# Performance work log

Hardware: AMD Instinct MI355X
Metric: run time of the kernel (lower is better)

Reference implementation:

```python
import jax, jax.numpy as jnp
import numpy as np

NUM_HEADS = 16
ROPE_THETA = 10000.0


def _rope_cos_sin(seq_len, head_dim, dtype):
    # Llama rotary embedding: inv_freq over even dims, emb = cat(freqs, freqs)
    inv_freq = 1.0 / (ROPE_THETA ** (jnp.arange(0, head_dim, 2, dtype=jnp.float32) / head_dim))
    t = jnp.arange(seq_len, dtype=jnp.float32)
    freqs = jnp.outer(t, inv_freq)              # [S, hd/2]
    emb = jnp.concatenate([freqs, freqs], -1)   # [S, hd]
    return jnp.cos(emb).astype(dtype), jnp.sin(emb).astype(dtype)


def _rotate_half(x):
    h = x.shape[-1] // 2
    return jnp.concatenate([-x[..., h:], x[..., :h]], axis=-1)


def setup_inputs() -> dict:
    key = jax.random.key(0)
    ks = jax.random.split(key, 5)
    B, S, D = 1, 2048, 2048
    scale = 0.02
    return {
        "hidden_states": jax.random.normal(ks[0], (B, S, D), jnp.float32),
        "Wq": jax.random.normal(ks[1], (D, D), jnp.float32) * scale,
        "Wk": jax.random.normal(ks[2], (D, D), jnp.float32) * scale,
        "Wv": jax.random.normal(ks[3], (D, D), jnp.float32) * scale,
        "Wo": jax.random.normal(ks[4], (D, D), jnp.float32) * scale,
    }


def reference(hidden_states, Wq, Wk, Wv, Wo):
    B, S, D = hidden_states.shape
    H = NUM_HEADS
    hd = D // H
    sm_scale = 1.0 / np.sqrt(hd)

    # QKV projections (nn.Linear without bias: x @ W.T), kept in [B,S,H,hd]
    q = (hidden_states @ Wq.T).reshape(B, S, H, hd)
    k = (hidden_states @ Wk.T).reshape(B, S, H, hd)
    v = (hidden_states @ Wv.T).reshape(B, S, H, hd)

    # RoPE (offset=0, no kv cache)
    cos, sin = _rope_cos_sin(S, hd, hidden_states.dtype)
    cos = cos[None, :, None, :]  # [1,S,1,hd]
    sin = sin[None, :, None, :]
    q = q * cos + _rotate_half(q) * sin
    k = k * cos + _rotate_half(k) * sin

    # Causal self-attention (exact math of FlashSelfAttention(causal=True))
    scores = jnp.einsum("bshd,bthd->bhst", q, k) * sm_scale  # [B,H,S,S]
    causal = jnp.tril(jnp.ones((S, S), dtype=bool))
    scores = jnp.where(causal[None, None], scores, jnp.finfo(scores.dtype).min)
    probs = jax.nn.softmax(scores, axis=-1)
    attn = jnp.einsum("bhst,bthd->bshd", probs, v)           # [B,S,H,hd]

    # Output projection
    attn = attn.reshape(B, S, H * hd)
    return attn @ Wo.T
```

## Files before the change

### kernel.cpp

```cpp
#include <hip/hip_runtime.h>
#include <hip/hip_bf16.h>
#include <math.h>

#define S_LEN 2048
#define DMODEL 2048
#define NHEADS 16
#define HDIM 128

typedef __bf16 bf16x8 __attribute__((ext_vector_type(8)));
typedef float f32x4 __attribute__((ext_vector_type(4)));
typedef float f32x16 __attribute__((ext_vector_type(16)));

__device__ __forceinline__ unsigned short f2b(float f) {
  union { float f; unsigned u; } c; c.f = f;
  unsigned r = (c.u + 0x7fffu + ((c.u >> 16) & 1u)) >> 16;
  return (unsigned short)r;
}
__device__ __forceinline__ float b2f(unsigned short b) {
  union { unsigned u; float f; } c; c.u = ((unsigned)b) << 16;
  return c.f;
}

__device__ __forceinline__ void gload_lds16(const unsigned short* g, unsigned short* l) {
  __builtin_amdgcn_global_load_lds(
      (__attribute__((address_space(1))) void*)(void*)g,
      (__attribute__((address_space(3))) void*)(void*)l, 16, 0, 0);
}

__global__ void cvt5_f32_bf16_k(const float* __restrict__ s0,
                                const float* __restrict__ s1,
                                const float* __restrict__ s2,
                                const float* __restrict__ s3,
                                const float* __restrict__ s4,
                                unsigned short* __restrict__ d0,
                                unsigned short* __restrict__ d1,
                                unsigned short* __restrict__ d2,
                                unsigned short* __restrict__ d3,
                                unsigned short* __restrict__ d4) {
  int gi = blockIdx.x * blockDim.x + threadIdx.x;
  int seg = gi >> 20;
  int i = (gi & 0xFFFFF) * 4;
  const float* src = (seg == 0) ? s0 : (seg == 1) ? s1 : (seg == 2) ? s2
                     : (seg == 3) ? s3 : s4;
  unsigned short* dst = (seg == 0) ? d0 : (seg == 1) ? d1 : (seg == 2) ? d2
                        : (seg == 3) ? d3 : d4;
  float4 v = *reinterpret_cast<const float4*>(src + i);
  ushort4 o;
  o.x = f2b(v.x); o.y = f2b(v.y); o.z = f2b(v.z); o.w = f2b(v.w);
  *reinterpret_cast<ushort4*>(dst + i) = o;
}

__global__ void rope_table_k(float* __restrict__ cs, float* __restrict__ sn) {
  int idx = blockIdx.x * blockDim.x + threadIdx.x;
  int s = idx >> 6, i = idx & 63;
  float inv = powf(10000.0f, -(float)(2 * i) / 128.0f);
  float a = (float)s * inv;
  cs[idx] = cosf(a);
  sn[idx] = sinf(a);
}

__global__ void rope_apply_k(unsigned short* __restrict__ q,
                             unsigned short* __restrict__ k,
                             const float* __restrict__ cs,
                             const float* __restrict__ sn) {
  const float SC = 0.08838834764831845f * 1.4426950408889634f;
  int idx = blockIdx.x * blockDim.x + threadIdx.x;
  int i = idx & 63;
  int h = (idx >> 6) & (NHEADS - 1);
  int s = idx >> 10;
  size_t base = (size_t)s * DMODEL + h * HDIM;
  float c = cs[s * 64 + i], sv = sn[s * 64 + i];
  float qc = c * SC, qs = sv * SC;
  float q1 = b2f(q[base + i]), q2 = b2f(q[base + i + 64]);
  q[base + i]      = f2b(q1 * qc - q2 * qs);
  q[base + i + 64] = f2b(q2 * qc + q1 * qs);
  float k1 = b2f(k[base + i]), k2 = b2f(k[base + i + 64]);
  k[base + i]      = f2b(k1 * c - k2 * sv);
  k[base + i + 64] = f2b(k2 * c + k1 * sv);
}

__global__ __launch_bounds__(256) void transpose_bf16_k(
    const unsigned short* __restrict__ in, unsigned short* __restrict__ out) {
  __shared__ unsigned short tile[64][72];
  int bx = blockIdx.x, by = blockIdx.y;
  int t = threadIdx.x;
#pragma unroll
  for (int i = 0; i < 2; ++i) {
    int ch = i * 256 + t;
    int r = ch >> 3, c8 = ch & 7;
    bf16x8 v = *reinterpret_cast<const bf16x8*>(
        in + (size_t)(by * 64 + r) * DMODEL + bx * 64 + c8 * 8);
    *reinterpret_cast<bf16x8*>(&tile[r][c8 * 8]) = v;
  }
  __syncthreads();
#pragma unroll
  for (int i = 0; i < 2; ++i) {
    int ch = i * 256 + t;
    int c = ch >> 3, r8 = ch & 7;
    union { bf16x8 v; unsigned short u[8]; } w;
#pragma unroll
    for (int j = 0; j < 8; ++j) w.u[j] = tile[r8 * 8 + j][c];
    *reinterpret_cast<bf16x8*>(
        out + (size_t)(bx * 64 + c) * S_LEN + by * 64 + r8 * 8) = w.v;
  }
}


#define MIDBAR_SEQ()                                      \
  do {                                                    \
    asm volatile("" ::: "memory");                        \
    __builtin_amdgcn_s_barrier();                         \
    asm volatile("s_waitcnt lgkmcnt(0)" ::: "memory");    \
    __builtin_amdgcn_sched_barrier(0);                    \
    __builtin_amdgcn_s_setprio(1);                        \
  } while (0)

#define ENDBAR_SEQ()                                      \
  do {                                                    \
    __builtin_amdgcn_s_setprio(0);                        \
    asm volatile("" ::: "memory");                        \
    __builtin_amdgcn_s_barrier();                         \
    asm volatile("" ::: "memory");                        \
  } while (0)

#define READA(QM)                                                              \
  do {                                                                         \
    _Pragma("unroll") for (int j = 0; j < MQ; ++j)                             \
    _Pragma("unroll") for (int kk = 0; kk < 2; ++kk) {                         \
      int row = wm * (BM / 2) + ((QM) * MQ + j) * 16 + li;                     \
      int c = (kk * 4 + g) ^ (li & 7);                                         \
      af[j][kk] = *reinterpret_cast<const bf16x8*>(&As[cur][row * 64 + c * 8]);\
    }                                                                          \
  } while (0)

#define READB(BF, QN)                                                          \
  do {                                                                         \
    _Pragma("unroll") for (int jn = 0; jn < 2; ++jn)                           \
    _Pragma("unroll") for (int kk = 0; kk < 2; ++kk) {                         \
      int row = wn * 64 + ((QN) * 2 + jn) * 16 + li;                           \
      int c = (kk * 4 + g) ^ (li & 7);                                         \
      BF[jn][kk] = *reinterpret_cast<const bf16x8*>(&Bs[cur][row * 64 + c * 8]);\
    }                                                                          \
  } while (0)

#define QUAD(QM, QN, BF)                                                       \
  do {                                                                         \
    _Pragma("unroll") for (int j = 0; j < MQ; ++j)                             \
    _Pragma("unroll") for (int jn = 0; jn < 2; ++jn)                           \
    _Pragma("unroll") for (int kk = 0; kk < 2; ++kk)                           \
      acc[(QM) * MQ + j][(QN) * 2 + jn] =                                      \
          __builtin_amdgcn_mfma_f32_16x16x32_bf16(                             \
              af[j][kk], BF[jn][kk], acc[(QM) * MQ + j][(QN) * 2 + jn], 0, 0, 0);\
  } while (0)

template <int BM, bool OUT_F32>
__global__ __launch_bounds__(512, 2) void gemm_8ph_k(
    const unsigned short* __restrict__ A, const unsigned short* __restrict__ B0p,
    const unsigned short* __restrict__ B1p, const unsigned short* __restrict__ B2p,
    void* __restrict__ C0, void* __restrict__ C1, void* __restrict__ C2,
    int M, int N, int K) {
  constexpr int MQ = BM / 64;
  constexpr int MR = BM / 32;

  __shared__ unsigned short As[2][BM * 64];
  __shared__ unsigned short Bs[2][256 * 64];

  const unsigned short* Bp = (blockIdx.z == 0) ? B0p : (blockIdx.z == 1) ? B1p : B2p;
  void* Cout = (blockIdx.z == 0) ? C0 : (blockIdx.z == 1) ? C1 : C2;

  int nwg = gridDim.x, bid = blockIdx.x;
  int wg = (bid & 7) * (nwg >> 3) + (bid >> 3);
  int ntn = N >> 8;
  int tm = wg / ntn, tn = wg % ntn;
  int m0 = tm * BM, n0 = tn << 8;

  const int tid = threadIdx.x;
  const int wave = tid >> 6, lane = tid & 63;
  const int g = lane >> 4, li = lane & 15;
  const int wm = wave >> 2, wn = wave & 3;

  auto stageB = [&](int buf, int tt, int qn) {
#pragma unroll
    for (int i = 0; i < 2; ++i) {
      int j = i * 512 + tid;
      int piece = j >> 8, rowin = (j >> 3) & 31, c = j & 7;
      int row = piece * 64 + qn * 32 + rowin;
      gload_lds16(Bp + (size_t)(n0 + row) * K + tt * 64 + ((c ^ (row & 7)) * 8),
                  &Bs[buf][row * 64 + c * 8]);
    }
  };
  auto stageA = [&](int buf, int tt, int qm) {
#pragma unroll
    for (int i = 0; i < BM / 128; ++i) {
      int j = i * 512 + tid;
      int piece = j / (2 * BM);
      int rowin = (j >> 3) & (BM / 4 - 1);
      int c = j & 7;
      int row = piece * (BM / 2) + qm * (BM / 4) + rowin;
      gload_lds16(A + (size_t)(m0 + row) * K + tt * 64 + ((c ^ (row & 7)) * 8),
                  &As[buf][row * 64 + c * 8]);
    }
  };

  f32x4 acc[MR][4];
#pragma unroll
  for (int i = 0; i < MR; ++i)
#pragma unroll
    for (int j = 0; j < 4; ++j) acc[i][j] = (f32x4){0.f, 0.f, 0.f, 0.f};

  const int nK = K >> 6;

  stageB(0, 0, 0); stageA(0, 0, 0); stageB(0, 0, 1); stageA(0, 0, 1);
  stageB(1, 1, 0); stageA(1, 1, 0); stageB(1, 1, 1); stageA(1, 1, 1);
  if constexpr (BM == 256) asm volatile("s_waitcnt vmcnt(8)" ::: "memory");
  else                     asm volatile("s_waitcnt vmcnt(6)" ::: "memory");
  asm volatile("" ::: "memory");
  __builtin_amdgcn_s_barrier();
  asm volatile("" ::: "memory");

  for (int t = 0; t < nK; ++t) {
    int cur = t & 1;
    bool pf = (t + 2 < nK);
    bf16x8 af[MQ][2], bf0[2][2], bf1[2][2];
    READA(0);
    READB(bf0, 0);
    MIDBAR_SEQ();
    QUAD(0, 0, bf0);
    ENDBAR_SEQ();
    READB(bf1, 1);
    if (pf) { stageB(cur, t + 2, 0); stageA(cur, t + 2, 0); }
    MIDBAR_SEQ();
    QUAD(0, 1, bf1);
    ENDBAR_SEQ();
    READA(1);
    if (pf) stageB(cur, t + 2, 1);
    MIDBAR_SEQ();
    QUAD(1, 1, bf1);
    ENDBAR_SEQ();
    if (pf) {
      stageA(cur, t + 2, 1);
      if constexpr (BM == 256) asm volatile("s_waitcnt vmcnt(8)" ::: "memory");
      else                     asm volatile("s_waitcnt vmcnt(6)" ::: "memory");
    } else {
      asm volatile("s_waitcnt vmcnt(0)" ::: "memory");
    }
    MIDBAR_SEQ();
    QUAD(1, 0, bf0);
    ENDBAR_SEQ();
  }

#pragma unroll
  for (int m = 0; m < MR; ++m) {
#pragma unroll
    for (int n = 0; n < 4; ++n) {
      int row = m0 + wm * (BM / 2) + m * 16 + g * 4;
      int col = n0 + wn * 64 + n * 16 + li;
#pragma unroll
      for (int r = 0; r < 4; ++r) {
        if (OUT_F32)
          reinterpret_cast<float*>(Cout)[(size_t)(row + r) * N + col] = acc[m][n][r];
        else
          reinterpret_cast<unsigned short*>(Cout)[(size_t)(row + r) * N + col] =
              f2b(acc[m][n][r]);
      }
    }
  }
}

#undef MIDBAR_SEQ
#undef ENDBAR_SEQ
#undef READA
#undef READB
#undef QUAD

__global__ __launch_bounds__(256) void flash_attn_k(
    const unsigned short* __restrict__ q, const unsigned short* __restrict__ k,
    const unsigned short* __restrict__ vt, unsigned short* __restrict__ o) {
  __shared__ unsigned short Ks[2][2][64 * 128];
  __shared__ unsigned short Vs[2][2][128 * 64];

  int L = blockIdx.x;
  int xcd = L & 7, j = L >> 3;
  int h = 2 * xcd + (j & 1);
  int qt = (j < 32) ? (31 - (j >> 1)) : ((j - 32) >> 1);

  int t = threadIdx.x, wave = t >> 6, l = t & 63;
  int l5 = l >> 5, l31 = l & 31;
  int par = wave >> 1, qh = wave & 1;
  int q0 = qt * 64;
  int q_abs = q0 + qh * 32 + l31;

  const unsigned short* vth = vt + (size_t)h * HDIM * S_LEN;

  auto stage = [&](int buf, int itv) {
#pragma unroll
    for (int p2 = 0; p2 < 2; ++p2) {
      int kv0 = (2 * itv + p2) * 64;
#pragma unroll
      for (int i = 0; i < 4; ++i) {
        int ch = i * 256 + t;
        int row = ch >> 4, c = ch & 15;
        gload_lds16(k + (size_t)(kv0 + row) * DMODEL + h * HDIM + ((c ^ (row & 7)) * 8),
                    &Ks[p2][buf][ch * 8]);
      }
#pragma unroll
      for (int i = 0; i < 4; ++i) {
        int ch = i * 256 + t;
        int row = ch >> 3, c = ch & 7;
        gload_lds16(vth + (size_t)row * S_LEN + kv0 + ((c ^ (row & 7)) * 8),
                    &Vs[p2][buf][ch * 8]);
      }
    }
  };

  bf16x8 qf[8];
#pragma unroll
  for (int kb = 0; kb < 8; ++kb)
    qf[kb] = *reinterpret_cast<const bf16x8*>(
        q + (size_t)q_abs * DMODEL + h * HDIM + kb * 16 + l5 * 8);

  f32x16 OT[4];
#pragma unroll
  for (int nf = 0; nf < 4; ++nf)
#pragma unroll
    for (int r = 0; r < 16; ++r) OT[nf][r] = 0.f;
  float m_r = -1e30f, l_r = 0.f;

  int nIter = (qt >> 1) + 1;
  stage(0, 0);

  for (int it = 0; it < nIter; ++it) {
    int cur = it & 1;
    if (it + 1 < nIter) {
      stage(cur ^ 1, it + 1);
      asm volatile("s_waitcnt vmcnt(16)" ::: "memory");
    } else {
      asm volatile("s_waitcnt vmcnt(0)" ::: "memory");
    }
    __builtin_amdgcn_s_barrier();
    asm volatile("" ::: "memory");

    int myt = 2 * it + par;
    if (myt <= qt) {
      int kv0 = myt * 64;
      f32x16 sf[2];
#pragma unroll
      for (int kvs = 0; kvs < 2; ++kvs)
#pragma unroll
        for (int r = 0; r < 16; ++r) sf[kvs][r] = 0.f;
#pragma unroll
      for (int kb = 0; kb < 8; ++kb) {
#pragma unroll
        for (int kvs = 0; kvs < 2; ++kvs) {
          int row = kvs * 32 + l31;
          int c = (2 * kb + l5) ^ (row & 7);
          bf16x8 kf = *reinterpret_cast<const bf16x8*>(&Ks[par][cur][row * 128 + c * 8]);
          sf[kvs] = __builtin_amdgcn_mfma_f32_32x32x16_bf16(kf, qf[kb], sf[kvs], 0, 0, 0);
        }
      }
      if (myt == qt) {
#pragma unroll
        for (int kvs = 0; kvs < 2; ++kvs)
#pragma unroll
          for (int r = 0; r < 16; ++r) {
            int kv_abs = kv0 + kvs * 32 + (r & 3) + 8 * (r >> 2) + 4 * l5;
            if (kv_abs > q_abs) sf[kvs][r] = -1e30f;
          }
      }
      float pm = -1e30f;
#pragma unroll
      for (int kvs = 0; kvs < 2; ++kvs)
#pragma unroll
        for (int r = 0; r < 16; ++r) pm = fmaxf(pm, sf[kvs][r]);
      pm = fmaxf(pm, __shfl_xor(pm, 32));
      float nm = fmaxf(m_r, pm);
      float alpha = exp2f(m_r - nm);
      m_r = nm;
      float ls = 0.f;
#pragma unroll
      for (int kvs = 0; kvs < 2; ++kvs)
#pragma unroll
        for (int r = 0; r < 16; ++r) {
          float pv = exp2f(sf[kvs][r] - nm);
          sf[kvs][r] = pv;
          ls += pv;
        }
      l_r = l_r * alpha + ls + __shfl_xor(ls, 32);
#pragma unroll
      for (int nf = 0; nf < 4; ++nf)
#pragma unroll
        for (int r = 0; r < 16; ++r) OT[nf][r] *= alpha;

      bf16x8 pf[4];
#pragma unroll
      for (int ks = 0; ks < 4; ++ks) {
        const int kvs = ks >> 1;
        const int m0 = 8 * (ks & 1);
        unsigned A0, A1, B0, B1;
        asm("v_cvt_pk_bf16_f32 %0, %1, %2" : "=v"(A0) : "v"(sf[kvs][m0 + 0]), "v"(sf[kvs][m0 + 1]));
        asm("v_cvt_pk_bf16_f32 %0, %1, %2" : "=v"(A1) : "v"(sf[kvs][m0 + 2]), "v"(sf[kvs][m0 + 3]));
        asm("v_cvt_pk_bf16_f32 %0, %1, %2" : "=v"(B0) : "v"(sf[kvs][m0 + 4]), "v"(sf[kvs][m0 + 5]));
        asm("v_cvt_pk_bf16_f32 %0, %1, %2" : "=v"(B1) : "v"(sf[kvs][m0 + 6]), "v"(sf[kvs][m0 + 7]));
        unsigned rA0 = (unsigned)__shfl_xor((int)A0, 32);
        unsigned rA1 = (unsigned)__shfl_xor((int)A1, 32);
        unsigned rB0 = (unsigned)__shfl_xor((int)B0, 32);
        unsigned rB1 = (unsigned)__shfl_xor((int)B1, 32);
        union { unsigned u[4]; bf16x8 v; } pk;
        pk.u[0] = l5 ? rB0 : A0;
        pk.u[1] = l5 ? rB1 : A1;
        pk.u[2] = l5 ? B0 : rA0;
        pk.u[3] = l5 ? B1 : rA1;
        pf[ks] = pk.v;
      }

#pragma unroll
      for (int ks = 0; ks < 4; ++ks) {
#pragma unroll
        for (int nf = 0; nf < 4; ++nf) {
          int row = nf * 32 + l31;
          int c = (2 * ks + l5) ^ (row & 7);
          bf16x8 vf = *reinterpret_cast<const bf16x8*>(&Vs[par][cur][row * 64 + c * 8]);
          OT[nf] = __builtin_amdgcn_mfma_f32_32x32x16_bf16(vf, pf[ks], OT[nf], 0, 0, 0);
        }
      }
    }
    __builtin_amdgcn_s_barrier();
    asm volatile("" ::: "memory");
  }

  float* MS = (float*)&Ks[0][0][0];
  float* ML = MS + 8192;
  if (par == 1) {
#pragma unroll
    for (int nf = 0; nf < 4; ++nf)
#pragma unroll
      for (int r = 0; r < 16; ++r) {
        int d = nf * 32 + (r & 3) + 8 * (r >> 2) + 4 * l5;
        MS[qh * 4096 + d * 32 + l31] = OT[nf][r];
      }
    if (l < 32) { ML[qh * 64 + l31] = m_r; ML[qh * 64 + 32 + l31] = l_r; }
  }
  __builtin_amdgcn_s_barrier();
  asm volatile("" ::: "memory");
  if (par == 0) {
    float mB = ML[qh * 64 + l31], lB = ML[qh * 64 + 32 + l31];
    float ms = fmaxf(m_r, mB);
    float eA = exp2f(m_r - ms), eB = exp2f(mB - ms);
    float inv = 1.0f / (l_r * eA + lB * eB);
#pragma unroll
    for (int nf = 0; nf < 4; ++nf)
#pragma unroll
      for (int r = 0; r < 16; ++r) {
        int d = nf * 32 + (r & 3) + 8 * (r >> 2) + 4 * l5;
        OT[nf][r] = (OT[nf][r] * eA + MS[qh * 4096 + d * 32 + l31] * eB) * inv;
      }
  }
  __builtin_amdgcn_s_barrier();
  asm volatile("" ::: "memory");
  if (par == 0) {
#pragma unroll
    for (int nf = 0; nf < 4; ++nf)
#pragma unroll
      for (int r = 0; r < 16; ++r) {
        int d = nf * 32 + (r & 3) + 8 * (r >> 2) + 4 * l5;
        MS[qh * 4096 + d * 32 + l31] = OT[nf][r];
      }
  }
  __builtin_amdgcn_s_barrier();
  asm volatile("" ::: "memory");
  {
    int qq = t >> 2;
    int dg = (t & 3) * 32;
    const float* src = MS + (qq >> 5) * 4096 + (qq & 31);
    unsigned pk[16];
#pragma unroll
    for (int i = 0; i < 16; ++i) {
      unsigned lo = f2b(src[(dg + 2 * i) * 32]);
      unsigned hi = f2b(src[(dg + 2 * i + 1) * 32]);
      pk[i] = lo | (hi << 16);
    }
    unsigned short* op = o + (size_t)(q0 + qq) * DMODEL + h * HDIM + dg;
#pragma unroll
    for (int i = 0; i < 4; ++i) {
      uint4 w = make_uint4(pk[4 * i], pk[4 * i + 1], pk[4 * i + 2], pk[4 * i + 3]);
      *reinterpret_cast<uint4*>(op + i * 8) = w;
    }
  }
}

extern "C" void kernel_launch(void* const* d_in, const int* in_sizes, int n_in,
                              void* d_out, int out_size, void* d_ws, size_t ws_size,
                              hipStream_t stream) {
  const float* hs = (const float*)d_in[0];
  const float* Wq = (const float*)d_in[1];
  const float* Wk = (const float*)d_in[2];
  const float* Wv = (const float*)d_in[3];
  const float* Wo = (const float*)d_in[4];

  char* ws = (char*)d_ws;
  const size_t MB = 1024 * 1024;
  unsigned short* hs_b = (unsigned short*)(ws + 0 * MB);
  unsigned short* Wq_b = (unsigned short*)(ws + 8 * MB);
  unsigned short* Wk_b = (unsigned short*)(ws + 16 * MB);
  unsigned short* Wv_b = (unsigned short*)(ws + 24 * MB);
  unsigned short* Wo_b = (unsigned short*)(ws + 32 * MB);
  unsigned short* qb = (unsigned short*)(ws + 40 * MB);
  unsigned short* kb = (unsigned short*)(ws + 48 * MB);
  unsigned short* vb = (unsigned short*)(ws + 56 * MB);
  unsigned short* ab = (unsigned short*)(ws + 64 * MB);
  float* cs = (float*)(ws + 72 * MB);
  float* sn = (float*)(ws + 72 * MB + 512 * 1024);
  unsigned short* vtb = hs_b;

  cvt5_f32_bf16_k<<<(5 * 1024 * 1024) / 256, 256, 0, stream>>>(
      hs, Wq, Wk, Wv, Wo, hs_b, Wq_b, Wk_b, Wv_b, Wo_b);

  rope_table_k<<<(S_LEN * 64) / 256, 256, 0, stream>>>(cs, sn);

  gemm_8ph_k<256, false><<<dim3(64, 1, 3), 512, 0, stream>>>(
      hs_b, Wq_b, Wk_b, Wv_b, qb, kb, vb, 2048, 2048, 2048);

  transpose_bf16_k<<<dim3(32, 32), 256, 0, stream>>>(vb, vtb);

  rope_apply_k<<<(S_LEN * NHEADS * 64) / 256, 256, 0, stream>>>(qb, kb, cs, sn);

  flash_attn_k<<<dim3(512), 256, 0, stream>>>(qb, kb, vtb, ab);

  gemm_8ph_k<128, true><<<dim3(128, 1, 1), 512, 0, stream>>>(
      ab, Wo_b, Wo_b, Wo_b, d_out, d_out, d_out, 2048, 2048, 2048);
}
```

Before: 215.3 us.

## Give each wave an independent 32-row query slice with private KV staging

Reworks the flash attention kernel so each of the four waves owns its own 32-row query slice, paired from both ends of the causal range so work is balanced. Each wave stages its own 32-wide K/V tiles into a private LDS region, which removes the block-wide barriers and the cross-wave softmax merge. The grid halves to 256 blocks. Blocks now read K/V redundantly per wave instead of sharing tiles, so global and L2 traffic rises, and occupancy may shift because fewer blocks are launched.

After: 252.1 us. +17.1%, slower.

```diff
diff --git a/kernel.cpp b/kernel.cpp
--- a/kernel.cpp
+++ b/kernel.cpp
@@ -276,40 +276,39 @@
 __global__ __launch_bounds__(256) void flash_attn_k(
     const unsigned short* __restrict__ q, const unsigned short* __restrict__ k,
     const unsigned short* __restrict__ vt, unsigned short* __restrict__ o) {
-  __shared__ unsigned short Ks[2][2][64 * 128];
-  __shared__ unsigned short Vs[2][2][128 * 64];
-
-  int L = blockIdx.x;
-  int xcd = L & 7, j = L >> 3;
-  int h = 2 * xcd + (j & 1);
-  int qt = (j < 32) ? (31 - (j >> 1)) : ((j - 32) >> 1);
+  __shared__ unsigned short lds[4][2][8192];
+
+  int bk = blockIdx.x;
+  int h = bk & 15;
+  int g = bk >> 4;
 
   int t = threadIdx.x, wave = t >> 6, l = t & 63;
   int l5 = l >> 5, l31 = l & 31;
-  int par = wave >> 1, qh = wave & 1;
-  int q0 = qt * 64;
-  int q_abs = q0 + qh * 32 + l31;
+  int sl = (wave == 0) ? 2 * g : (wave == 1) ? 2 * g + 1
+           : (wave == 2) ? 62 - 2 * g : 63 - 2 * g;
+  int q0w = sl * 32;
+  int q_abs = q0w + l31;
+  int nt = sl + 1;
 
   const unsigned short* vth = vt + (size_t)h * HDIM * S_LEN;
 
-  auto stage = [&](int buf, int itv) {
-#pragma unroll
-    for (int p2 = 0; p2 < 2; ++p2) {
-      int kv0 = (2 * itv + p2) * 64;
-#pragma unroll
-      for (int i = 0; i < 4; ++i) {
-        int ch = i * 256 + t;
-        int row = ch >> 4, c = ch & 15;
-        gload_lds16(k + (size_t)(kv0 + row) * DMODEL + h * HDIM + ((c ^ (row & 7)) * 8),
-                    &Ks[p2][buf][ch * 8]);
-      }
-#pragma unroll
-      for (int i = 0; i < 4; ++i) {
-        int ch = i * 256 + t;
-        int row = ch >> 3, c = ch & 7;
-        gload_lds16(vth + (size_t)row * S_LEN + kv0 + ((c ^ (row & 7)) * 8),
-                    &Vs[p2][buf][ch * 8]);
-      }
+  auto stage = [&](int buf, int tt) {
+    int kv0 = tt * 32;
+    unsigned short* Kb = &lds[wave][buf][0];
+    unsigned short* Vb = &lds[wave][buf][4096];
+#pragma unroll
+    for (int i = 0; i < 8; ++i) {
+      int ch = i * 64 + l;
+      int row = ch >> 4, c = ch & 15;
+      gload_lds16(k + (size_t)(kv0 + row) * DMODEL + h * HDIM + ((c ^ (row & 7)) * 8),
+                  Kb + ch * 8);
+    }
+#pragma unroll
+    for (int i = 0; i < 8; ++i) {
+      int ch = i * 64 + l;
+      int row = ch >> 2, c = ch & 3;
+      gload_lds16(vth + (size_t)row * S_LEN + kv0 + ((c ^ (row & 3)) * 8),
+                  Vb + ch * 8);
     }
   };
 
@@ -326,164 +325,110 @@
     for (int r = 0; r < 16; ++r) OT[nf][r] = 0.f;
   float m_r = -1e30f, l_r = 0.f;
 
-  int nIter = (qt >> 1) + 1;
   stage(0, 0);
 
-  for (int it = 0; it < nIter; ++it) {
-    int cur = it & 1;
-    if (it + 1 < nIter) {
-      stage(cur ^ 1, it + 1);
+  for (int tt = 0; tt < nt; ++tt) {
+    int cur = tt & 1;
+    if (tt + 1 < nt) {
+      stage(cur ^ 1, tt + 1);
       asm volatile("s_waitcnt vmcnt(16)" ::: "memory");
     } else {
       asm volatile("s_waitcnt vmcnt(0)" ::: "memory");
     }
-    __builtin_amdgcn_s_barrier();
-    asm volatile("" ::: "memory");
-
-    int myt = 2 * it + par;
-    if (myt <= qt) {
-      int kv0 = myt * 64;
-      f32x16 sf[2];
-#pragma unroll
-      for (int kvs = 0; kvs < 2; ++kvs)
-#pragma unroll
-        for (int r = 0; r < 16; ++r) sf[kvs][r] = 0.f;
-#pragma unroll
-      for (int kb = 0; kb < 8; ++kb) {
-#pragma unroll
-        for (int kvs = 0; kvs < 2; ++kvs) {
-          int row = kvs * 32 + l31;
-          int c = (2 * kb + l5) ^ (row & 7);
-          bf16x8 kf = *reinterpret_cast<const bf16x8*>(&Ks[par][cur][row * 128 + c * 8]);
-          sf[kvs] = __builtin_amdgcn_mfma_f32_32x32x16_bf16(kf, qf[kb], sf[kvs], 0, 0, 0);
-        }
+    __builtin_amdgcn_sched_barrier(0);
+
+    int kv0 = tt * 32;
+    const unsigned short* Kb = &lds[wave][cur][0];
+    const unsigned short* Vb = &lds[wave][cur][4096];
+
+    f32x16 sf;
+#pragma unroll
+    for (int r = 0; r < 16; ++r) sf[r] = 0.f;
+#pragma unroll
+    for (int kb = 0; kb < 8; ++kb) {
+      int c = (2 * kb + l5) ^ (l31 & 7);
+      bf16x8 kf = *reinterpret_cast<const bf16x8*>(Kb + (l31 * 16 + c) * 8);
+      sf = __builtin_amdgcn_mfma_f32_32x32x16_bf16(kf, qf[kb], sf, 0, 0, 0);
+    }
+    if (tt == nt - 1) {
+#pragma unroll
+      for (int r = 0; r < 16; ++r) {
+        int kv_abs = kv0 + (r & 3) + 8 * (r >> 2) + 4 * l5;
+        if (kv_abs > q_abs) sf[r] = -1e30f;
       }
-      if (myt == qt) {
-#pragma unroll
-        for (int kvs = 0; kvs < 2; ++kvs)
-#pragma unroll
-          for (int r = 0; r < 16; ++r) {
-            int kv_abs = kv0 + kvs * 32 + (r & 3) + 8 * (r >> 2) + 4 * l5;
-            if (kv_abs > q_abs) sf[kvs][r] = -1e30f;
-          }
+    }
+    float pm = -1e30f;
+#pragma unroll
+    for (int r = 0; r < 16; ++r) pm = fmaxf(pm, sf[r]);
+    pm = fmaxf(pm, __shfl_xor(pm, 32));
+    float nm = fmaxf(m_r, pm);
+    float alpha = exp2f(m_r - nm);
+    m_r = nm;
+    float ls = 0.f;
+#pragma unroll
+    for (int r = 0; r < 16; ++r) {
+      float pv = exp2f(sf[r] - nm);
+      sf[r] = pv;
+      ls += pv;
+    }
+    l_r = l_r * alpha + ls + __shfl_xor(ls, 32);
+#pragma unroll
+    for (int nf = 0; nf < 4; ++nf)
+#pragma unroll
+      for (int r = 0; r < 16; ++r) OT[nf][r] *= alpha;
+
+    bf16x8 pf[2];
+#pragma unroll
+    for (int ks = 0; ks < 2; ++ks) {
+      const int m0 = 8 * ks;
+      unsigned A0, A1, B0, B1;
+      asm("v_cvt_pk_bf16_f32 %0, %1, %2" : "=v"(A0) : "v"(sf[m0 + 0]), "v"(sf[m0 + 1]));
+      asm("v_cvt_pk_bf16_f32 %0, %1, %2" : "=v"(A1) : "v"(sf[m0 + 2]), "v"(sf[m0 + 3]));
+      asm("v_cvt_pk_bf16_f32 %0, %1, %2" : "=v"(B0) : "v"(sf[m0 + 4]), "v"(sf[m0 + 5]));
+      asm("v_cvt_pk_bf16_f32 %0, %1, %2" : "=v"(B1) : "v"(sf[m0 + 6]), "v"(sf[m0 + 7]));
+      unsigned rA0 = (unsigned)__shfl_xor((int)A0, 32);
+      unsigned rA1 = (unsigned)__shfl_xor((int)A1, 32);
+      unsigned rB0 = (unsigned)__shfl_xor((int)B0, 32);
+      unsigned rB1 = (unsigned)__shfl_xor((int)B1, 32);
+      union { unsigned u[4]; bf16x8 v; } pk;
+      pk.u[0] = l5 ? rB0 : A0;
+      pk.u[1] = l5 ? rB1 : A1;
+      pk.u[2] = l5 ? B0 : rA0;
+      pk.u[3] = l5 ? B1 : rA1;
+      pf[ks] = pk.v;
+    }
+
+#pragma unroll
+    for (int ks = 0; ks < 2; ++ks) {
+#pragma unroll
+      for (int nf = 0; nf < 4; ++nf) {
+        int row = nf * 32 + l31;
+        int c = (2 * ks + l5) ^ (row & 3);
+        bf16x8 vf = *reinterpret_cast<const bf16x8*>(Vb + (row * 4 + c) * 8);
+        OT[nf] = __builtin_amdgcn_mfma_f32_32x32x16_bf16(vf, pf[ks], OT[nf], 0, 0, 0);
       }
-      float pm = -1e30f;
-#pragma unroll
-      for (int kvs = 0; kvs < 2; ++kvs)
-#pragma unroll
-        for (int r = 0; r < 16; ++r) pm = fmaxf(pm, sf[kvs][r]);
-      pm = fmaxf(pm, __shfl_xor(pm, 32));
-      float nm = fmaxf(m_r, pm);
-      float alpha = exp2f(m_r - nm);
-      m_r = nm;
-      float ls = 0.f;
-#pragma unroll
-      for (int kvs = 0; kvs < 2; ++kvs)
-#pragma unroll
-        for (int r = 0; r < 16; ++r) {
-          float pv = exp2f(sf[kvs][r] - nm);
-          sf[kvs][r] = pv;
-          ls += pv;
-        }
-      l_r = l_r * alpha + ls + __shfl_xor(ls, 32);
-#pragma unroll
-      for (int nf = 0; nf < 4; ++nf)
-#pragma unroll
-        for (int r = 0; r < 16; ++r) OT[nf][r] *= alpha;
-
-      bf16x8 pf[4];
-#pragma unroll
-      for (int ks = 0; ks < 4; ++ks) {
-        const int kvs = ks >> 1;
-        const int m0 = 8 * (ks & 1);
-        unsigned A0, A1, B0, B1;
-        asm("v_cvt_pk_bf16_f32 %0, %1, %2" : "=v"(A0) : "v"(sf[kvs][m0 + 0]), "v"(sf[kvs][m0 + 1]));
-        asm("v_cvt_pk_bf16_f32 %0, %1, %2" : "=v"(A1) : "v"(sf[kvs][m0 + 2]), "v"(sf[kvs][m0 + 3]));
-        asm("v_cvt_pk_bf16_f32 %0, %1, %2" : "=v"(B0) : "v"(sf[kvs][m0 + 4]), "v"(sf[kvs][m0 + 5]));
-        asm("v_cvt_pk_bf16_f32 %0, %1, %2" : "=v"(B1) : "v"(sf[kvs][m0 + 6]), "v"(sf[kvs][m0 + 7]));
-        unsigned rA0 = (unsigned)__shfl_xor((int)A0, 32);
-        unsigned rA1 = (unsigned)__shfl_xor((int)A1, 32);
-        unsigned rB0 = (unsigned)__shfl_xor((int)B0, 32);
-        unsigned rB1 = (unsigned)__shfl_xor((int)B1, 32);
-        union { unsigned u[4]; bf16x8 v; } pk;
-        pk.u[0] = l5 ? rB0 : A0;
-        pk.u[1] = l5 ? rB1 : A1;
-        pk.u[2] = l5 ? B0 : rA0;
-        pk.u[3] = l5 ? B1 : rA1;
-        pf[ks] = pk.v;
-      }
-
-#pragma unroll
-      for (int ks = 0; ks < 4; ++ks) {
-#pragma unroll
-        for (int nf = 0; nf < 4; ++nf) {
-          int row = nf * 32 + l31;
-          int c = (2 * ks + l5) ^ (row & 7);
-          bf16x8 vf = *reinterpret_cast<const bf16x8*>(&Vs[par][cur][row * 64 + c * 8]);
-          OT[nf] = __builtin_amdgcn_mfma_f32_32x32x16_bf16(vf, pf[ks], OT[nf], 0, 0, 0);
-        }
-      }
-    }
-    __builtin_amdgcn_s_barrier();
-    asm volatile("" ::: "memory");
-  }
-
-  float* MS = (float*)&Ks[0][0][0];
-  float* ML = MS + 8192;
-  if (par == 1) {
+    }
+  }
+
+  {
+    unsigned short* Tb = &lds[wave][0][0];
+    float inv = 1.0f / l_r;
 #pragma unroll
     for (int nf = 0; nf < 4; ++nf)
 #pragma unroll
       for (int r = 0; r < 16; ++r) {
         int d = nf * 32 + (r & 3) + 8 * (r >> 2) + 4 * l5;
-        MS[qh * 4096 + d * 32 + l31] = OT[nf][r];
+        Tb[l31 * 136 + d] = f2b(OT[nf][r] * inv);
       }
-    if (l < 32) { ML[qh * 64 + l31] = m_r; ML[qh * 64 + 32 + l31] = l_r; }
-  }
-  __builtin_amdgcn_s_barrier();
-  asm volatile("" ::: "memory");
-  if (par == 0) {
-    float mB = ML[qh * 64 + l31], lB = ML[qh * 64 + 32 + l31];
-    float ms = fmaxf(m_r, mB);
-    float eA = exp2f(m_r - ms), eB = exp2f(mB - ms);
-    float inv = 1.0f / (l_r * eA + lB * eB);
-#pragma unroll
-    for (int nf = 0; nf < 4; ++nf)
-#pragma unroll
-      for (int r = 0; r < 16; ++r) {
-        int d = nf * 32 + (r & 3) + 8 * (r >> 2) + 4 * l5;
-        OT[nf][r] = (OT[nf][r] * eA + MS[qh * 4096 + d * 32 + l31] * eB) * inv;
-      }
-  }
-  __builtin_amdgcn_s_barrier();
-  asm volatile("" ::: "memory");
-  if (par == 0) {
-#pragma unroll
-    for (int nf = 0; nf < 4; ++nf)
-#pragma unroll
-      for (int r = 0; r < 16; ++r) {
-        int d = nf * 32 + (r & 3) + 8 * (r >> 2) + 4 * l5;
-        MS[qh * 4096 + d * 32 + l31] = OT[nf][r];
-      }
-  }
-  __builtin_amdgcn_s_barrier();
-  asm volatile("" ::: "memory");
-  {
-    int qq = t >> 2;
-    int dg = (t & 3) * 32;
-    const float* src = MS + (qq >> 5) * 4096 + (qq & 31);
-    unsigned pk[16];
-#pragma unroll
-    for (int i = 0; i < 16; ++i) {
-      unsigned lo = f2b(src[(dg + 2 * i) * 32]);
-      unsigned hi = f2b(src[(dg + 2 * i + 1) * 32]);
-      pk[i] = lo | (hi << 16);
-    }
-    unsigned short* op = o + (size_t)(q0 + qq) * DMODEL + h * HDIM + dg;
-#pragma unroll
-    for (int i = 0; i < 4; ++i) {
-      uint4 w = make_uint4(pk[4 * i], pk[4 * i + 1], pk[4 * i + 2], pk[4 * i + 3]);
-      *reinterpret_cast<uint4*>(op + i * 8) = w;
+    asm volatile("s_waitcnt lgkmcnt(0)" ::: "memory");
+    __builtin_amdgcn_sched_barrier(0);
+#pragma unroll
+    for (int i = 0; i < 8; ++i) {
+      int ch = i * 64 + l;
+      int row = ch >> 4, c = ch & 15;
+      bf16x8 v = *reinterpret_cast<const bf16x8*>(Tb + row * 136 + c * 8);
+      *reinterpret_cast<bf16x8*>(
+          o + (size_t)(q0w + row) * DMODEL + h * HDIM + c * 8) = v;
     }
   }
 }
@@ -524,7 +469,7 @@
 
   rope_apply_k<<<(S_LEN * NHEADS * 64) / 256, 256, 0, stream>>>(qb, kb, cs, sn);
 
-  flash_attn_k<<<dim3(512), 256, 0, stream>>>(qb, kb, vtb, ab);
+  flash_attn_k<<<dim3(256), 256, 0, stream>>>(qb, kb, vtb, ab);
 
   gemm_8ph_k<128, true><<<dim3(128, 1, 1), 512, 0, stream>>>(
       ab, Wo_b, Wo_b, Wo_b, d_out, d_out, d_out, 2048, 2048, 2048);
```
